# Kernel optimization log

Measured on AMD Instinct MI355X. Metric: run time of the kernel, lower is better.

The kernel has to match this reference:

```python
import jax, jax.numpy as jnp
import numpy as np

NUM_HEADS = 8

def setup_inputs() -> dict:
    key = jax.random.key(0)
    ks = jax.random.split(key, 6)
    B, S, D, K = 2, 2048, 512, 64
    x = jax.random.normal(ks[0], (B, S, D), dtype=jnp.float32)
    routes = jax.random.randint(ks[1], (S, K), 0, S, dtype=jnp.int32)
    distances = jax.random.uniform(ks[2], (S, S), dtype=jnp.float32)
    W_in = jax.random.normal(ks[3], (D, D), dtype=jnp.float32) * (1.0 / np.sqrt(D))
    W_out = jax.random.normal(ks[4], (D, D), dtype=jnp.float32) * (1.0 / np.sqrt(D))
    b_out = jnp.zeros((D,), dtype=jnp.float32)
    return {"x": x, "routes": routes, "distances": distances,
            "W_in": W_in, "W_out": W_out, "b_out": b_out}

def reference(x, routes, distances, W_in, W_out, b_out):
    # x: [B,S,D]; routes: [S,K] int gather table; distances: [S,S]
    B, S, D = x.shape
    H = NUM_HEADS
    hd = D // H
    K = routes.shape[1]
    # in_proj (torch Linear, no bias): y = x @ W^T
    h = jnp.einsum('bsd,ed->bse', x, W_in).reshape(B, S, H, hd)
    # gather fusion windows via precomputed routes: [B,S,K,H,hd]
    gathered = h[:, routes]
    # weighted fusion: weights from precomputed Cantor distance matrix
    d = jnp.take_along_axis(distances, routes.astype(jnp.int32), axis=1)  # [S,K]
    w = jax.nn.softmax(-d, axis=-1)  # normalized fusion weights
    fused = jnp.einsum('sk,bskhd->bshd', w, gathered)  # [B,S,H,hd]
    fused = fused.reshape(B, S, D)
    # out_proj + residual (dropout is identity in eval)
    out = jnp.einsum('bsd,ed->bse', fused, W_out) + b_out
    return out + x
```

## Files before the change

### kernel.cpp

```cpp
#include <hip/hip_runtime.h>
#include <hip/hip_bf16.h>

#define S_DIM 2048
#define D_DIM 512
#define B_DIM 2
#define K_RT  64
#define M_DIM 4096

typedef __attribute__((ext_vector_type(8))) short short8;
typedef __attribute__((ext_vector_type(4))) float f32x4;
typedef unsigned int u32;
#define AS1 __attribute__((address_space(1)))
#define AS3 __attribute__((address_space(3)))

static __device__ __forceinline__ float bf16lo_to_f(unsigned u) {
    union { unsigned u; float f; } c; c.u = u << 16; return c.f;
}
static __device__ __forceinline__ float bf16hi_to_f(unsigned u) {
    union { unsigned u; float f; } c; c.u = u & 0xffff0000u; return c.f;
}
static __device__ __forceinline__ unsigned short f_to_bf16(float f) {
    union { float f; unsigned u; } c; c.f = f;
    unsigned u = c.u;
    u += 0x7fffu + ((u >> 16) & 1u);
    return (unsigned short)(u >> 16);
}
static __device__ __forceinline__ unsigned pk2(float a, float b) {
    return (unsigned)f_to_bf16(a) | ((unsigned)f_to_bf16(b) << 16);
}

__global__ __launch_bounds__(256) void prep_cast(
    const float* __restrict__ x, const float* __restrict__ Wi, const float* __restrict__ Wo,
    unsigned short* __restrict__ xb, unsigned short* __restrict__ wib,
    unsigned short* __restrict__ wob)
{
    const int g = blockIdx.x * 256 + threadIdx.x;
    const int NX = M_DIM * D_DIM / 4;
    const int NW = D_DIM * D_DIM / 4;
    const float* src; unsigned short* dst; int off;
    if (g < NX)           { src = x;  dst = xb;  off = g; }
    else if (g < NX + NW) { src = Wi; dst = wib; off = g - NX; }
    else                  { src = Wo; dst = wob; off = g - NX - NW; }
    const float4 v = ((const float4*)src)[off];
    ushort4 o;
    o.x = f_to_bf16(v.x); o.y = f_to_bf16(v.y);
    o.z = f_to_bf16(v.z); o.w = f_to_bf16(v.w);
    ((ushort4*)dst)[off] = o;
}

#define GBM 64
#define GBN 64
#define GBK 64

template<bool OUTF32>
__global__ __launch_bounds__(256) void gemm_bt(
    const unsigned short* __restrict__ A,
    const unsigned short* __restrict__ B,
    void* __restrict__ Cv,
    const float* __restrict__ bias, const float* __restrict__ residual,
    int M, int N, int K)
{
    __shared__ unsigned short As[2][GBM * 32];
    __shared__ unsigned short Bs[2][GBN * 32];

    const int tid  = threadIdx.x;
    const int lane = tid & 63;
    const int wv   = tid >> 6;
    const int wm   = (wv & 1) * 32;
    const int wn   = (wv >> 1) * 32;
    const int m0   = blockIdx.y * GBM;
    const int n0   = blockIdx.x * GBN;

    const int srow  = wv * 16 + (lane >> 2);
    const int skoff = (lane & 3) * 8;

    const int mi = lane & 15;
    const int kg = lane >> 4;

    f32x4 acc[2][2] = {};

    for (int k0 = 0; k0 < K; k0 += GBK) {
        const size_t arow = (size_t)(m0 + srow) * K + k0 + skoff;
        const size_t brow = (size_t)(n0 + srow) * K + k0 + skoff;
        __builtin_amdgcn_global_load_lds((const AS1 u32*)(A + arow),
                                         (AS3 u32*)(As[0] + wv * 512), 16, 0, 0);
        __builtin_amdgcn_global_load_lds((const AS1 u32*)(A + arow + 32),
                                         (AS3 u32*)(As[1] + wv * 512), 16, 0, 0);
        __builtin_amdgcn_global_load_lds((const AS1 u32*)(B + brow),
                                         (AS3 u32*)(Bs[0] + wv * 512), 16, 0, 0);
        __builtin_amdgcn_global_load_lds((const AS1 u32*)(B + brow + 32),
                                         (AS3 u32*)(Bs[1] + wv * 512), 16, 0, 0);
        __syncthreads();

        #pragma unroll
        for (int kh = 0; kh < 2; ++kh) {
            short8 af0 = *(const short8*)(As[kh] + (wm +      mi) * 32 + kg * 8);
            short8 af1 = *(const short8*)(As[kh] + (wm + 16 + mi) * 32 + kg * 8);
            short8 bf0 = *(const short8*)(Bs[kh] + (wn +      mi) * 32 + kg * 8);
            short8 bf1 = *(const short8*)(Bs[kh] + (wn + 16 + mi) * 32 + kg * 8);

            acc[0][0] = __builtin_amdgcn_mfma_f32_16x16x32_bf16(af0, bf0, acc[0][0], 0, 0, 0);
            acc[0][1] = __builtin_amdgcn_mfma_f32_16x16x32_bf16(af0, bf1, acc[0][1], 0, 0, 0);
            acc[1][0] = __builtin_amdgcn_mfma_f32_16x16x32_bf16(af1, bf0, acc[1][0], 0, 0, 0);
            acc[1][1] = __builtin_amdgcn_mfma_f32_16x16x32_bf16(af1, bf1, acc[1][1], 0, 0, 0);
        }
        __syncthreads();
    }

    const int rb  = (lane >> 4) * 4;
    const int col = lane & 15;
    #pragma unroll
    for (int i = 0; i < 2; ++i) {
        #pragma unroll
        for (int j = 0; j < 2; ++j) {
            #pragma unroll
            for (int r = 0; r < 4; ++r) {
                const int m = m0 + wm + i * 16 + rb + r;
                const int n = n0 + wn + j * 16 + col;
                const float v = acc[i][j][r];
                if (OUTF32) {
                    ((float*)Cv)[(size_t)m * N + n] = v + bias[n] + residual[(size_t)m * N + n];
                } else {
                    ((unsigned short*)Cv)[(size_t)m * N + n] = f_to_bf16(v);
                }
            }
        }
    }
}

__global__ __launch_bounds__(256) void fuse_gather(
    const unsigned short* __restrict__ h, const int* __restrict__ routes,
    const float* __restrict__ distances, unsigned short* __restrict__ fused)
{
    const int tid  = threadIdx.x;
    const int lane = tid & 63;
    const int wv   = tid >> 6;
    const int bx   = blockIdx.x;
    const int b    = bx & 1;
    const int s    = (bx >> 1) * 4 + wv;

    const int rt = routes[s * K_RT + lane];
    const float v = -distances[(size_t)s * S_DIM + rt];
    float mx = v;
    #pragma unroll
    for (int off = 32; off >= 1; off >>= 1) mx = fmaxf(mx, __shfl_xor(mx, off, 64));
    const float e = __expf(v - mx);
    float sum = e;
    #pragma unroll
    for (int off = 32; off >= 1; off >>= 1) sum += __shfl_xor(sum, off, 64);
    const float wl = e / sum;

    const unsigned short* hb = h + (size_t)b * S_DIM * D_DIM;
    float acc[8] = {};
    #pragma unroll
    for (int k = 0; k < 64; ++k) {
        const int   rk = __builtin_amdgcn_readlane(rt, k);
        const float wk = __int_as_float(__builtin_amdgcn_readlane(__float_as_int(wl), k));
        const uint4 p = *(const uint4*)(hb + (size_t)rk * D_DIM + lane * 8);
        acc[0] = fmaf(wk, bf16lo_to_f(p.x), acc[0]);
        acc[1] = fmaf(wk, bf16hi_to_f(p.x), acc[1]);
        acc[2] = fmaf(wk, bf16lo_to_f(p.y), acc[2]);
        acc[3] = fmaf(wk, bf16hi_to_f(p.y), acc[3]);
        acc[4] = fmaf(wk, bf16lo_to_f(p.z), acc[4]);
        acc[5] = fmaf(wk, bf16hi_to_f(p.z), acc[5]);
        acc[6] = fmaf(wk, bf16lo_to_f(p.w), acc[6]);
        acc[7] = fmaf(wk, bf16hi_to_f(p.w), acc[7]);
    }
    uint4 o;
    o.x = pk2(acc[0], acc[1]);
    o.y = pk2(acc[2], acc[3]);
    o.z = pk2(acc[4], acc[5]);
    o.w = pk2(acc[6], acc[7]);
    *(uint4*)(fused + ((size_t)b * S_DIM + s) * D_DIM + lane * 8) = o;
}

extern "C" void kernel_launch(void* const* d_in, const int* in_sizes, int n_in,
                              void* d_out, int out_size, void* d_ws, size_t ws_size,
                              hipStream_t stream) {
    const float* x         = (const float*)d_in[0];
    const int*   routes    = (const int*)  d_in[1];
    const float* distances = (const float*)d_in[2];
    const float* W_in      = (const float*)d_in[3];
    const float* W_out     = (const float*)d_in[4];
    const float* b_out     = (const float*)d_in[5];
    float* out = (float*)d_out;

    unsigned short* xb  = (unsigned short*)d_ws;
    unsigned short* wib = xb  + (size_t)M_DIM * D_DIM;
    unsigned short* wob = wib + (size_t)D_DIM * D_DIM;
    unsigned short* hb  = wob + (size_t)D_DIM * D_DIM;
    unsigned short* fb  = hb  + (size_t)M_DIM * D_DIM;

    const dim3 ggrid(D_DIM / GBN, M_DIM / GBM);

    prep_cast<<<2560, 256, 0, stream>>>(x, W_in, W_out, xb, wib, wob);
    gemm_bt<false><<<ggrid, 256, 0, stream>>>(xb, wib, hb, nullptr, nullptr, M_DIM, D_DIM, D_DIM);
    fuse_gather<<<dim3(1024), 256, 0, stream>>>(hb, routes, distances, fb);
    gemm_bt<true><<<ggrid, 256, 0, stream>>>(fb, wob, out, b_out, x, M_DIM, D_DIM, D_DIM);
}
```

Baseline: 112.9 us.

## Merge all four stages into one cooperative persistent kernel with grid syncs

Replaces the four separate launches (cast, in-proj GEMM, gather-fuse, out-proj GEMM) with a single cooperative kernel of 512 blocks that steps through the stages, separated by grid-wide syncs. The GEMM tile loop gains double-buffered LDS staging so the next K-slice loads while MFMAs run. Tiles are remapped per block for locality. This removes per-kernel launch gaps and tail effects, at the cost of grid-barrier overhead and fewer resident blocks per stage (512 blocks doing the gather that previously used 1024).

```diff
diff --git a/kernel.cpp b/kernel.cpp
--- a/kernel.cpp
+++ b/kernel.cpp
@@ -1,5 +1,7 @@
 #include <hip/hip_runtime.h>
-#include <hip/hip_bf16.h>
+#include <hip/hip_cooperative_groups.h>
+
+namespace cg = cooperative_groups;
 
 #define S_DIM 2048
 #define D_DIM 512
@@ -7,6 +9,11 @@
 #define K_RT  64
 #define M_DIM 4096
 
+#define NBLK  512
+#define GBM 64
+#define GBN 64
+#define GBK 64
+
 typedef __attribute__((ext_vector_type(8))) short short8;
 typedef __attribute__((ext_vector_type(4))) float f32x4;
 typedef unsigned int u32;
@@ -29,75 +36,55 @@
     return (unsigned)f_to_bf16(a) | ((unsigned)f_to_bf16(b) << 16);
 }
 
-__global__ __launch_bounds__(256) void prep_cast(
-    const float* __restrict__ x, const float* __restrict__ Wi, const float* __restrict__ Wo,
-    unsigned short* __restrict__ xb, unsigned short* __restrict__ wib,
-    unsigned short* __restrict__ wob)
-{
-    const int g = blockIdx.x * 256 + threadIdx.x;
-    const int NX = M_DIM * D_DIM / 4;
-    const int NW = D_DIM * D_DIM / 4;
-    const float* src; unsigned short* dst; int off;
-    if (g < NX)           { src = x;  dst = xb;  off = g; }
-    else if (g < NX + NW) { src = Wi; dst = wib; off = g - NX; }
-    else                  { src = Wo; dst = wob; off = g - NX - NW; }
-    const float4 v = ((const float4*)src)[off];
-    ushort4 o;
-    o.x = f_to_bf16(v.x); o.y = f_to_bf16(v.y);
-    o.z = f_to_bf16(v.z); o.w = f_to_bf16(v.w);
-    ((ushort4*)dst)[off] = o;
-}
-
-#define GBM 64
-#define GBN 64
-#define GBK 64
-
 template<bool OUTF32>
-__global__ __launch_bounds__(256) void gemm_bt(
+static __device__ __forceinline__ void gemm_bt_block(
     const unsigned short* __restrict__ A,
     const unsigned short* __restrict__ B,
     void* __restrict__ Cv,
     const float* __restrict__ bias, const float* __restrict__ residual,
-    int M, int N, int K)
+    unsigned short (*As)[GBM * 32], unsigned short (*Bs)[GBN * 32],
+    int tile, int lane, int wv)
 {
-    __shared__ unsigned short As[2][GBM * 32];
-    __shared__ unsigned short Bs[2][GBN * 32];
-
-    const int tid  = threadIdx.x;
-    const int lane = tid & 63;
-    const int wv   = tid >> 6;
-    const int wm   = (wv & 1) * 32;
-    const int wn   = (wv >> 1) * 32;
-    const int m0   = blockIdx.y * GBM;
-    const int n0   = blockIdx.x * GBN;
+    const int N = D_DIM, K = D_DIM;
+    const int n0 = (tile & 7) * GBN;
+    const int m0 = (tile >> 3) * GBM;
+    const int wm = (wv & 1) * 32;
+    const int wn = (wv >> 1) * 32;
 
     const int srow  = wv * 16 + (lane >> 2);
     const int skoff = (lane & 3) * 8;
+    const unsigned short* Arow = A + (size_t)(m0 + srow) * K + skoff;
+    const unsigned short* Brow = B + (size_t)(n0 + srow) * K + skoff;
 
     const int mi = lane & 15;
     const int kg = lane >> 4;
 
     f32x4 acc[2][2] = {};
 
-    for (int k0 = 0; k0 < K; k0 += GBK) {
-        const size_t arow = (size_t)(m0 + srow) * K + k0 + skoff;
-        const size_t brow = (size_t)(n0 + srow) * K + k0 + skoff;
-        __builtin_amdgcn_global_load_lds((const AS1 u32*)(A + arow),
-                                         (AS3 u32*)(As[0] + wv * 512), 16, 0, 0);
-        __builtin_amdgcn_global_load_lds((const AS1 u32*)(A + arow + 32),
-                                         (AS3 u32*)(As[1] + wv * 512), 16, 0, 0);
-        __builtin_amdgcn_global_load_lds((const AS1 u32*)(B + brow),
-                                         (AS3 u32*)(Bs[0] + wv * 512), 16, 0, 0);
-        __builtin_amdgcn_global_load_lds((const AS1 u32*)(B + brow + 32),
-                                         (AS3 u32*)(Bs[1] + wv * 512), 16, 0, 0);
-        __syncthreads();
-
+#define STAGE(buf, k0) do {                                                              \
+    __builtin_amdgcn_global_load_lds((const AS1 u32*)(Arow + (k0)),                      \
+                                     (AS3 u32*)(As[(buf)*2 + 0] + wv * 512), 16, 0, 0);  \
+    __builtin_amdgcn_global_load_lds((const AS1 u32*)(Arow + (k0) + 32),                 \
+                                     (AS3 u32*)(As[(buf)*2 + 1] + wv * 512), 16, 0, 0);  \
+    __builtin_amdgcn_global_load_lds((const AS1 u32*)(Brow + (k0)),                      \
+                                     (AS3 u32*)(Bs[(buf)*2 + 0] + wv * 512), 16, 0, 0);  \
+    __builtin_amdgcn_global_load_lds((const AS1 u32*)(Brow + (k0) + 32),                 \
+                                     (AS3 u32*)(Bs[(buf)*2 + 1] + wv * 512), 16, 0, 0);  \
+} while (0)
+
+    STAGE(0, 0);
+    __syncthreads();
+
+    int cur = 0;
+    #pragma unroll
+    for (int t = 0; t < K / GBK; ++t) {
+        if (t + 1 < K / GBK) STAGE(cur ^ 1, (t + 1) * GBK);
         #pragma unroll
         for (int kh = 0; kh < 2; ++kh) {
-            short8 af0 = *(const short8*)(As[kh] + (wm +      mi) * 32 + kg * 8);
-            short8 af1 = *(const short8*)(As[kh] + (wm + 16 + mi) * 32 + kg * 8);
-            short8 bf0 = *(const short8*)(Bs[kh] + (wn +      mi) * 32 + kg * 8);
-            short8 bf1 = *(const short8*)(Bs[kh] + (wn + 16 + mi) * 32 + kg * 8);
+            short8 af0 = *(const short8*)(As[cur*2 + kh] + (wm +      mi) * 32 + kg * 8);
+            short8 af1 = *(const short8*)(As[cur*2 + kh] + (wm + 16 + mi) * 32 + kg * 8);
+            short8 bf0 = *(const short8*)(Bs[cur*2 + kh] + (wn +      mi) * 32 + kg * 8);
+            short8 bf1 = *(const short8*)(Bs[cur*2 + kh] + (wn + 16 + mi) * 32 + kg * 8);
 
             acc[0][0] = __builtin_amdgcn_mfma_f32_16x16x32_bf16(af0, bf0, acc[0][0], 0, 0, 0);
             acc[0][1] = __builtin_amdgcn_mfma_f32_16x16x32_bf16(af0, bf1, acc[0][1], 0, 0, 0);
@@ -105,7 +92,9 @@
             acc[1][1] = __builtin_amdgcn_mfma_f32_16x16x32_bf16(af1, bf1, acc[1][1], 0, 0, 0);
         }
         __syncthreads();
-    }
+        cur ^= 1;
+    }
+#undef STAGE
 
     const int rb  = (lane >> 4) * 4;
     const int col = lane & 15;
@@ -128,50 +117,96 @@
     }
 }
 
-__global__ __launch_bounds__(256) void fuse_gather(
-    const unsigned short* __restrict__ h, const int* __restrict__ routes,
-    const float* __restrict__ distances, unsigned short* __restrict__ fused)
+__global__ __launch_bounds__(256, 2) void fused_pipeline(
+    const float* __restrict__ x, const int* __restrict__ routes,
+    const float* __restrict__ distances, const float* __restrict__ W_in,
+    const float* __restrict__ W_out, const float* __restrict__ b_out,
+    float* __restrict__ out,
+    unsigned short* __restrict__ xb, unsigned short* __restrict__ wib,
+    unsigned short* __restrict__ wob, unsigned short* __restrict__ hb,
+    unsigned short* __restrict__ fb)
 {
+    __shared__ unsigned short As[4][GBM * 32];
+    __shared__ unsigned short Bs[4][GBN * 32];
+
+    cg::grid_group grid = cg::this_grid();
+
     const int tid  = threadIdx.x;
+    const int bid  = blockIdx.x;
     const int lane = tid & 63;
     const int wv   = tid >> 6;
-    const int bx   = blockIdx.x;
-    const int b    = bx & 1;
-    const int s    = (bx >> 1) * 4 + wv;
-
-    const int rt = routes[s * K_RT + lane];
-    const float v = -distances[(size_t)s * S_DIM + rt];
-    float mx = v;
-    #pragma unroll
-    for (int off = 32; off >= 1; off >>= 1) mx = fmaxf(mx, __shfl_xor(mx, off, 64));
-    const float e = __expf(v - mx);
-    float sum = e;
-    #pragma unroll
-    for (int off = 32; off >= 1; off >>= 1) sum += __shfl_xor(sum, off, 64);
-    const float wl = e / sum;
-
-    const unsigned short* hb = h + (size_t)b * S_DIM * D_DIM;
-    float acc[8] = {};
-    #pragma unroll
-    for (int k = 0; k < 64; ++k) {
-        const int   rk = __builtin_amdgcn_readlane(rt, k);
-        const float wk = __int_as_float(__builtin_amdgcn_readlane(__float_as_int(wl), k));
-        const uint4 p = *(const uint4*)(hb + (size_t)rk * D_DIM + lane * 8);
-        acc[0] = fmaf(wk, bf16lo_to_f(p.x), acc[0]);
-        acc[1] = fmaf(wk, bf16hi_to_f(p.x), acc[1]);
-        acc[2] = fmaf(wk, bf16lo_to_f(p.y), acc[2]);
-        acc[3] = fmaf(wk, bf16hi_to_f(p.y), acc[3]);
-        acc[4] = fmaf(wk, bf16lo_to_f(p.z), acc[4]);
-        acc[5] = fmaf(wk, bf16hi_to_f(p.z), acc[5]);
-        acc[6] = fmaf(wk, bf16lo_to_f(p.w), acc[6]);
-        acc[7] = fmaf(wk, bf16hi_to_f(p.w), acc[7]);
-    }
-    uint4 o;
-    o.x = pk2(acc[0], acc[1]);
-    o.y = pk2(acc[2], acc[3]);
-    o.z = pk2(acc[4], acc[5]);
-    o.w = pk2(acc[6], acc[7]);
-    *(uint4*)(fused + ((size_t)b * S_DIM + s) * D_DIM + lane * 8) = o;
+
+    {
+        const int NX = M_DIM * D_DIM / 4;
+        const int NW = D_DIM * D_DIM / 4;
+        int g = bid * 256 + tid;
+        #pragma unroll
+        for (int it = 0; it < 5; ++it, g += NBLK * 256) {
+            const float* src; unsigned short* dst; int off;
+            if (g < NX)           { src = x;     dst = xb;  off = g; }
+            else if (g < NX + NW) { src = W_in;  dst = wib; off = g - NX; }
+            else                  { src = W_out; dst = wob; off = g - NX - NW; }
+            const float4 v = ((const float4*)src)[off];
+            ushort4 o;
+            o.x = f_to_bf16(v.x); o.y = f_to_bf16(v.y);
+            o.z = f_to_bf16(v.z); o.w = f_to_bf16(v.w);
+            ((ushort4*)dst)[off] = o;
+        }
+    }
+    __threadfence();
+    grid.sync();
+
+    const int tile = (bid & 7) * 64 + (bid >> 3);
+
+    gemm_bt_block<false>(xb, wib, hb, nullptr, nullptr, As, Bs, tile, lane, wv);
+    __threadfence();
+    grid.sync();
+
+    {
+        const int b      = bid & 1;
+        const int s_base = (bid >> 1) * 4 + wv;
+        const unsigned short* hbp = hb + (size_t)b * S_DIM * D_DIM;
+        #pragma unroll
+        for (int si = 0; si < 2; ++si) {
+            const int s  = s_base + si * 1024;
+            const int rt = routes[s * K_RT + lane];
+            const float v = -distances[(size_t)s * S_DIM + rt];
+            float mx = v;
+            #pragma unroll
+            for (int off = 32; off >= 1; off >>= 1) mx = fmaxf(mx, __shfl_xor(mx, off, 64));
+            const float e = __expf(v - mx);
+            float sum = e;
+            #pragma unroll
+            for (int off = 32; off >= 1; off >>= 1) sum += __shfl_xor(sum, off, 64);
+            const float wl = e / sum;
+
+            float acc[8] = {};
+            #pragma unroll
+            for (int k = 0; k < 64; ++k) {
+                const int   rk = __builtin_amdgcn_readlane(rt, k);
+                const float wk = __int_as_float(__builtin_amdgcn_readlane(__float_as_int(wl), k));
+                const uint4 p = *(const uint4*)(hbp + (size_t)rk * D_DIM + lane * 8);
+                acc[0] = fmaf(wk, bf16lo_to_f(p.x), acc[0]);
+                acc[1] = fmaf(wk, bf16hi_to_f(p.x), acc[1]);
+                acc[2] = fmaf(wk, bf16lo_to_f(p.y), acc[2]);
+                acc[3] = fmaf(wk, bf16hi_to_f(p.y), acc[3]);
+                acc[4] = fmaf(wk, bf16lo_to_f(p.z), acc[4]);
+                acc[5] = fmaf(wk, bf16hi_to_f(p.z), acc[5]);
+                acc[6] = fmaf(wk, bf16lo_to_f(p.w), acc[6]);
+                acc[7] = fmaf(wk, bf16hi_to_f(p.w), acc[7]);
+            }
+            uint4 o;
+            o.x = pk2(acc[0], acc[1]);
+            o.y = pk2(acc[2], acc[3]);
+            o.z = pk2(acc[4], acc[5]);
+            o.w = pk2(acc[6], acc[7]);
+            *(uint4*)(fb + ((size_t)b * S_DIM + s) * D_DIM + lane * 8) = o;
+        }
+    }
+    __threadfence();
+    grid.sync();
+
+    gemm_bt_block<true>(fb, wob, out, b_out, x, As, Bs, tile, lane, wv);
 }
 
 extern "C" void kernel_launch(void* const* d_in, const int* in_sizes, int n_in,
@@ -191,10 +226,11 @@
     unsigned short* hb  = wob + (size_t)D_DIM * D_DIM;
     unsigned short* fb  = hb  + (size_t)M_DIM * D_DIM;
 
-    const dim3 ggrid(D_DIM / GBN, M_DIM / GBM);
-
-    prep_cast<<<2560, 256, 0, stream>>>(x, W_in, W_out, xb, wib, wob);
-    gemm_bt<false><<<ggrid, 256, 0, stream>>>(xb, wib, hb, nullptr, nullptr, M_DIM, D_DIM, D_DIM);
-    fuse_gather<<<dim3(1024), 256, 0, stream>>>(hb, routes, distances, fb);
-    gemm_bt<true><<<ggrid, 256, 0, stream>>>(fb, wob, out, b_out, x, M_DIM, D_DIM, D_DIM);
-}
+    void* kargs[] = {
+        (void*)&x, (void*)&routes, (void*)&distances, (void*)&W_in,
+        (void*)&W_out, (void*)&b_out, (void*)&out,
+        (void*)&xb, (void*)&wib, (void*)&wob, (void*)&hb, (void*)&fb
+    };
+    hipLaunchCooperativeKernel(reinterpret_cast<void*>(fused_pipeline),
+                               dim3(NBLK), dim3(256), kargs, 0, stream);
+}
```

Result: slower. 436.5 us (+286.7%).

## Double-buffer GEMM LDS loads, swizzle blocks per XCD, split gather accumulators

Applied to the files above, without the earlier changes.

The GEMM now prefetches the next K tile into a second LDS buffer while computing the current one, with one barrier per step. Blocks are launched on a 1D grid and remapped so each XCD handles a contiguous 8x8 group of tiles, which should improve L2 reuse. The gather kernel splits its 64-route reduction into two independent accumulator chains and sets an occupancy hint. The cost is doubled LDS per block and more registers in the gather.

```diff
diff --git a/kernel.cpp b/kernel.cpp
--- a/kernel.cpp
+++ b/kernel.cpp
@@ -6,6 +6,10 @@
 #define B_DIM 2
 #define K_RT  64
 #define M_DIM 4096
+
+#define GBM 64
+#define GBN 64
+#define GBK 64
 
 typedef __attribute__((ext_vector_type(8))) short short8;
 typedef __attribute__((ext_vector_type(4))) float f32x4;
@@ -48,56 +52,61 @@
     ((ushort4*)dst)[off] = o;
 }
 
-#define GBM 64
-#define GBN 64
-#define GBK 64
-
 template<bool OUTF32>
 __global__ __launch_bounds__(256) void gemm_bt(
     const unsigned short* __restrict__ A,
     const unsigned short* __restrict__ B,
     void* __restrict__ Cv,
-    const float* __restrict__ bias, const float* __restrict__ residual,
-    int M, int N, int K)
+    const float* __restrict__ bias, const float* __restrict__ residual)
 {
-    __shared__ unsigned short As[2][GBM * 32];
-    __shared__ unsigned short Bs[2][GBN * 32];
-
+    __shared__ unsigned short As[4][GBM * 32];
+    __shared__ unsigned short Bs[4][GBN * 32];
+
+    const int N = D_DIM, K = D_DIM;
     const int tid  = threadIdx.x;
     const int lane = tid & 63;
     const int wv   = tid >> 6;
-    const int wm   = (wv & 1) * 32;
-    const int wn   = (wv >> 1) * 32;
-    const int m0   = blockIdx.y * GBM;
-    const int n0   = blockIdx.x * GBN;
+    const int bid  = blockIdx.x;
+    const int within = bid >> 3;
+    const int m0 = ((bid & 7) * 8 + (within >> 3)) * GBM;
+    const int n0 = (within & 7) * GBN;
+    const int wm = (wv & 1) * 32;
+    const int wn = (wv >> 1) * 32;
 
     const int srow  = wv * 16 + (lane >> 2);
     const int skoff = (lane & 3) * 8;
+    const unsigned short* Arow = A + (size_t)(m0 + srow) * K + skoff;
+    const unsigned short* Brow = B + (size_t)(n0 + srow) * K + skoff;
 
     const int mi = lane & 15;
     const int kg = lane >> 4;
 
     f32x4 acc[2][2] = {};
 
-    for (int k0 = 0; k0 < K; k0 += GBK) {
-        const size_t arow = (size_t)(m0 + srow) * K + k0 + skoff;
-        const size_t brow = (size_t)(n0 + srow) * K + k0 + skoff;
-        __builtin_amdgcn_global_load_lds((const AS1 u32*)(A + arow),
-                                         (AS3 u32*)(As[0] + wv * 512), 16, 0, 0);
-        __builtin_amdgcn_global_load_lds((const AS1 u32*)(A + arow + 32),
-                                         (AS3 u32*)(As[1] + wv * 512), 16, 0, 0);
-        __builtin_amdgcn_global_load_lds((const AS1 u32*)(B + brow),
-                                         (AS3 u32*)(Bs[0] + wv * 512), 16, 0, 0);
-        __builtin_amdgcn_global_load_lds((const AS1 u32*)(B + brow + 32),
-                                         (AS3 u32*)(Bs[1] + wv * 512), 16, 0, 0);
-        __syncthreads();
-
+#define STAGE(buf, k0) do {                                                              \
+    __builtin_amdgcn_global_load_lds((const AS1 u32*)(Arow + (k0)),                      \
+                                     (AS3 u32*)(As[(buf)*2 + 0] + wv * 512), 16, 0, 0);  \
+    __builtin_amdgcn_global_load_lds((const AS1 u32*)(Arow + (k0) + 32),                 \
+                                     (AS3 u32*)(As[(buf)*2 + 1] + wv * 512), 16, 0, 0);  \
+    __builtin_amdgcn_global_load_lds((const AS1 u32*)(Brow + (k0)),                      \
+                                     (AS3 u32*)(Bs[(buf)*2 + 0] + wv * 512), 16, 0, 0);  \
+    __builtin_amdgcn_global_load_lds((const AS1 u32*)(Brow + (k0) + 32),                 \
+                                     (AS3 u32*)(Bs[(buf)*2 + 1] + wv * 512), 16, 0, 0);  \
+} while (0)
+
+    STAGE(0, 0);
+    __syncthreads();
+
+    #pragma unroll
+    for (int t = 0; t < K / GBK; ++t) {
+        const int cur = t & 1;
+        if (t + 1 < K / GBK) STAGE(cur ^ 1, (t + 1) * GBK);
         #pragma unroll
         for (int kh = 0; kh < 2; ++kh) {
-            short8 af0 = *(const short8*)(As[kh] + (wm +      mi) * 32 + kg * 8);
-            short8 af1 = *(const short8*)(As[kh] + (wm + 16 + mi) * 32 + kg * 8);
-            short8 bf0 = *(const short8*)(Bs[kh] + (wn +      mi) * 32 + kg * 8);
-            short8 bf1 = *(const short8*)(Bs[kh] + (wn + 16 + mi) * 32 + kg * 8);
+            short8 af0 = *(const short8*)(As[cur*2 + kh] + (wm +      mi) * 32 + kg * 8);
+            short8 af1 = *(const short8*)(As[cur*2 + kh] + (wm + 16 + mi) * 32 + kg * 8);
+            short8 bf0 = *(const short8*)(Bs[cur*2 + kh] + (wn +      mi) * 32 + kg * 8);
+            short8 bf1 = *(const short8*)(Bs[cur*2 + kh] + (wn + 16 + mi) * 32 + kg * 8);
 
             acc[0][0] = __builtin_amdgcn_mfma_f32_16x16x32_bf16(af0, bf0, acc[0][0], 0, 0, 0);
             acc[0][1] = __builtin_amdgcn_mfma_f32_16x16x32_bf16(af0, bf1, acc[0][1], 0, 0, 0);
@@ -106,6 +115,7 @@
         }
         __syncthreads();
     }
+#undef STAGE
 
     const int rb  = (lane >> 4) * 4;
     const int col = lane & 15;
@@ -128,7 +138,7 @@
     }
 }
 
-__global__ __launch_bounds__(256) void fuse_gather(
+__global__ __launch_bounds__(256, 4) void fuse_gather(
     const unsigned short* __restrict__ h, const int* __restrict__ routes,
     const float* __restrict__ distances, unsigned short* __restrict__ fused)
 {
@@ -151,26 +161,37 @@
     const float wl = e / sum;
 
     const unsigned short* hb = h + (size_t)b * S_DIM * D_DIM;
-    float acc[8] = {};
-    #pragma unroll
-    for (int k = 0; k < 64; ++k) {
-        const int   rk = __builtin_amdgcn_readlane(rt, k);
-        const float wk = __int_as_float(__builtin_amdgcn_readlane(__float_as_int(wl), k));
-        const uint4 p = *(const uint4*)(hb + (size_t)rk * D_DIM + lane * 8);
-        acc[0] = fmaf(wk, bf16lo_to_f(p.x), acc[0]);
-        acc[1] = fmaf(wk, bf16hi_to_f(p.x), acc[1]);
-        acc[2] = fmaf(wk, bf16lo_to_f(p.y), acc[2]);
-        acc[3] = fmaf(wk, bf16hi_to_f(p.y), acc[3]);
-        acc[4] = fmaf(wk, bf16lo_to_f(p.z), acc[4]);
-        acc[5] = fmaf(wk, bf16hi_to_f(p.z), acc[5]);
-        acc[6] = fmaf(wk, bf16lo_to_f(p.w), acc[6]);
-        acc[7] = fmaf(wk, bf16hi_to_f(p.w), acc[7]);
+    float acc0[8] = {}, acc1[8] = {};
+    #pragma unroll
+    for (int k = 0; k < 32; ++k) {
+        const int   rk0 = __builtin_amdgcn_readlane(rt, k);
+        const int   rk1 = __builtin_amdgcn_readlane(rt, k + 32);
+        const float wk0 = __int_as_float(__builtin_amdgcn_readlane(__float_as_int(wl), k));
+        const float wk1 = __int_as_float(__builtin_amdgcn_readlane(__float_as_int(wl), k + 32));
+        const uint4 p0 = *(const uint4*)(hb + (size_t)rk0 * D_DIM + lane * 8);
+        const uint4 p1 = *(const uint4*)(hb + (size_t)rk1 * D_DIM + lane * 8);
+        acc0[0] = fmaf(wk0, bf16lo_to_f(p0.x), acc0[0]);
+        acc0[1] = fmaf(wk0, bf16hi_to_f(p0.x), acc0[1]);
+        acc0[2] = fmaf(wk0, bf16lo_to_f(p0.y), acc0[2]);
+        acc0[3] = fmaf(wk0, bf16hi_to_f(p0.y), acc0[3]);
+        acc0[4] = fmaf(wk0, bf16lo_to_f(p0.z), acc0[4]);
+        acc0[5] = fmaf(wk0, bf16hi_to_f(p0.z), acc0[5]);
+        acc0[6] = fmaf(wk0, bf16lo_to_f(p0.w), acc0[6]);
+        acc0[7] = fmaf(wk0, bf16hi_to_f(p0.w), acc0[7]);
+        acc1[0] = fmaf(wk1, bf16lo_to_f(p1.x), acc1[0]);
+        acc1[1] = fmaf(wk1, bf16hi_to_f(p1.x), acc1[1]);
+        acc1[2] = fmaf(wk1, bf16lo_to_f(p1.y), acc1[2]);
+        acc1[3] = fmaf(wk1, bf16hi_to_f(p1.y), acc1[3]);
+        acc1[4] = fmaf(wk1, bf16lo_to_f(p1.z), acc1[4]);
+        acc1[5] = fmaf(wk1, bf16hi_to_f(p1.z), acc1[5]);
+        acc1[6] = fmaf(wk1, bf16lo_to_f(p1.w), acc1[6]);
+        acc1[7] = fmaf(wk1, bf16hi_to_f(p1.w), acc1[7]);
     }
     uint4 o;
-    o.x = pk2(acc[0], acc[1]);
-    o.y = pk2(acc[2], acc[3]);
-    o.z = pk2(acc[4], acc[5]);
-    o.w = pk2(acc[6], acc[7]);
+    o.x = pk2(acc0[0] + acc1[0], acc0[1] + acc1[1]);
+    o.y = pk2(acc0[2] + acc1[2], acc0[3] + acc1[3]);
+    o.z = pk2(acc0[4] + acc1[4], acc0[5] + acc1[5]);
+    o.w = pk2(acc0[6] + acc1[6], acc0[7] + acc1[7]);
     *(uint4*)(fused + ((size_t)b * S_DIM + s) * D_DIM + lane * 8) = o;
 }
 
@@ -191,10 +212,8 @@
     unsigned short* hb  = wob + (size_t)D_DIM * D_DIM;
     unsigned short* fb  = hb  + (size_t)M_DIM * D_DIM;
 
-    const dim3 ggrid(D_DIM / GBN, M_DIM / GBM);
-
     prep_cast<<<2560, 256, 0, stream>>>(x, W_in, W_out, xb, wib, wob);
-    gemm_bt<false><<<ggrid, 256, 0, stream>>>(xb, wib, hb, nullptr, nullptr, M_DIM, D_DIM, D_DIM);
+    gemm_bt<false><<<512, 256, 0, stream>>>(xb, wib, hb, nullptr, nullptr);
     fuse_gather<<<dim3(1024), 256, 0, stream>>>(hb, routes, distances, fb);
-    gemm_bt<true><<<ggrid, 256, 0, stream>>>(fb, wob, out, b_out, x, M_DIM, D_DIM, D_DIM);
-}
+    gemm_bt<true><<<512, 256, 0, stream>>>(fb, wob, out, b_out, x);
+}
```

After: 116.6 us. 1.03x slower.
